# Kernel tuning notes

Measured on AMD Instinct MI355X. Metric: run time of the kernel, lower is better.

The kernel has to match this reference:

```python
import jax, jax.numpy as jnp
import numpy as np

NUM_USERS = 100000
NUM_ITEMS = 50000
EMB = 64
NNZ = 4_800_000
N = NUM_USERS + NUM_ITEMS


def setup_inputs() -> dict:
    key = jax.random.key(0)
    k1, k2, k3, k4, k5 = jax.random.split(key, 5)
    row = jax.random.randint(k1, (NNZ,), 0, N, dtype=jnp.int64 if jax.config.jax_enable_x64 else jnp.int32)
    col = jax.random.randint(k2, (NNZ,), 0, N, dtype=row.dtype)
    # normalized adjacency values (positive, ~1/avg_degree scale)
    vals = jax.random.uniform(k3, (NNZ,), dtype=jnp.float32) * (1.0 / 32.0)
    user_emb = jax.random.normal(k4, (NUM_USERS, EMB), dtype=jnp.float32)
    item_emb = jax.random.normal(k5, (NUM_ITEMS, EMB), dtype=jnp.float32)
    return {"row": row, "col": col, "vals": vals,
            "user_emb": user_emb, "item_emb": item_emb, "n_layers": 3}


def reference(row, col, vals, user_emb, item_emb, n_layers):
    # ego_embeddings = cat(user, item)  -> [N, D]
    ego = jnp.concatenate([user_emb, item_emb], axis=0)
    acc = ego  # running sum over layers (layer 0 included)
    for _ in range(n_layers):
        # sparse.mm(norm_adj, ego): gather source rows, scale, scatter-add to dest rows
        ego = jax.ops.segment_sum(vals[:, None] * ego[col], row, num_segments=N)
        acc = acc + ego
    mean_emb = acc / jnp.asarray(n_layers + 1, dtype=acc.dtype)  # mean over layer axis
    return mean_emb[:NUM_USERS], mean_emb[NUM_USERS:]
```

## Files before the change

kernel.cpp:

```cpp
#include <hip/hip_runtime.h>
#include <hip/hip_fp16.h>


#define NUSERS 100000
#define NITEMS 50000
#define NN     150000
#define D      64
#define NNZ_E  4800000

#define NB_BU  586
#define BU_PAD 592
#define NCHUNK 1024
#define CH     4688
#define STAGE_CAP 16384

__global__ void init_kernel(const float* __restrict__ ue,
                            const float* __restrict__ ie,
                            float* __restrict__ acc,
                            __half* __restrict__ ego) {
    int t = blockIdx.x * blockDim.x + threadIdx.x;
    const int total = NN * (D / 4);
    if (t >= total) return;
    const int user_f4 = NUSERS * (D / 4);
    float4 v;
    if (t < user_f4) v = ((const float4*)ue)[t];
    else             v = ((const float4*)ie)[t - user_f4];
    ((float4*)acc)[t] = v;
    __half2 h01 = __float22half2_rn(make_float2(v.x, v.y));
    __half2 h23 = __float22half2_rn(make_float2(v.z, v.w));
    uint2 packed;
    packed.x = *(unsigned*)&h01;
    packed.y = *(unsigned*)&h23;
    ((uint2*)ego)[t] = packed;
}

__global__ void p1_kernel(const int* __restrict__ row, int* __restrict__ cnt) {
    __shared__ int l[BU_PAD];
    for (int i = threadIdx.x; i < BU_PAD; i += 256) l[i] = 0;
    __syncthreads();
    int b = blockIdx.x;
    int beg = b * CH, end = min(beg + CH, NNZ_E);
    for (int e = beg + threadIdx.x; e < end; e += 256)
        atomicAdd(&l[row[e] >> 8], 1);
    __syncthreads();
    for (int i = threadIdx.x; i < BU_PAD; i += 256) cnt[b * BU_PAD + i] = l[i];
}

__global__ void s1_kernel(const int* __restrict__ cnt,
                          int* __restrict__ woff,
                          int* __restrict__ butot) {
    __shared__ int wsum[16];
    int bu = blockIdx.x;
    int c = threadIdx.x;
    int lane = c & 63;
    int w = c >> 6;
    int d = cnt[c * BU_PAD + bu];
    int incl = d;
    #pragma unroll
    for (int off = 1; off < 64; off <<= 1) {
        int t = __shfl_up(incl, off, 64);
        if (lane >= off) incl += t;
    }
    if (lane == 63) wsum[w] = incl;
    __syncthreads();
    int woffs = 0;
    for (int i = 0; i < w; ++i) woffs += wsum[i];
    woff[c * BU_PAD + bu] = woffs + incl - d;
    if (c == 1023) butot[bu] = woffs + incl;
}

__global__ void s2_kernel(const int* __restrict__ butot, int* __restrict__ bbase) {
    __shared__ int sh[1024];
    int t = threadIdx.x;
    sh[t] = (t < NB_BU) ? butot[t] : 0;
    __syncthreads();
    for (int off = 1; off < 1024; off <<= 1) {
        int x = (t >= off) ? sh[t - off] : 0;
        __syncthreads();
        sh[t] += x;
        __syncthreads();
    }
    if (t == 0) bbase[0] = 0;
    if (t < NB_BU) bbase[t + 1] = sh[t];
}

__global__ void p2_kernel(const int* __restrict__ row,
                          const int* __restrict__ col,
                          const float* __restrict__ vals,
                          const int* __restrict__ woff,
                          const int* __restrict__ bbase,
                          uint2* __restrict__ rec) {
    __shared__ int cur[BU_PAD];
    int b = blockIdx.x;
    for (int i = threadIdx.x; i < BU_PAD; i += 256) {
        int base = (i < NB_BU) ? bbase[i] : 0;
        cur[i] = base + woff[b * BU_PAD + i];
    }
    __syncthreads();
    int beg = b * CH, end = min(beg + CH, NNZ_E);
    for (int e = beg + threadIdx.x; e < end; e += 256) {
        int r = row[e];
        unsigned code = (unsigned)(vals[e] * 524288.0f + 0.5f);
        code = min(code, 16383u);
        unsigned cv = ((unsigned)col[e] << 14) | code;
        int p = atomicAdd(&cur[r >> 8], 1);
        rec[p] = make_uint2(cv, (unsigned)(r & 255));
    }
}

__global__ __launch_bounds__(512) void p3f_kernel(const int* __restrict__ bbase,
                                                  const uint2* __restrict__ rec,
                                                  int* __restrict__ start,
                                                  int* __restrict__ deg,
                                                  unsigned* __restrict__ ecv) {
    __shared__ unsigned stage[STAGE_CAP];
    __shared__ int lh[256];
    __shared__ int cur[256];
    __shared__ int wsum[4];
    int bu = blockIdx.x;
    int beg = bbase[bu], end = bbase[bu + 1];
    int t = threadIdx.x;
    if (t < 256) lh[t] = 0;
    __syncthreads();
    for (int i = beg + t; i < end; i += 512)
        atomicAdd(&lh[rec[i].y], 1);
    __syncthreads();
    int h = 0, incl = 0;
    int lane = t & 63, w = t >> 6;
    if (t < 256) {
        h = lh[t];
        incl = h;
        #pragma unroll
        for (int off = 1; off < 64; off <<= 1) {
            int x = __shfl_up(incl, off, 64);
            if (lane >= off) incl += x;
        }
        if (lane == 63) wsum[w] = incl;
    }
    __syncthreads();
    if (t < 256) {
        int woffs = 0;
        for (int i = 0; i < w; ++i) woffs += wsum[i];
        int excl = woffs + incl - h;
        cur[t] = excl;
        int n0 = (bu << 8) + t;
        if (n0 < NN) {
            start[n0] = beg + excl;
            deg[n0] = h;
        }
    }
    __syncthreads();
    for (int i = beg + t; i < end; i += 512) {
        uint2 r = rec[i];
        int p = atomicAdd(&cur[r.y], 1);
        stage[p] = r.x;
    }
    __syncthreads();
    int n_edges = end - beg;
    for (int i = t; i < n_edges; i += 512)
        ecv[beg + i] = stage[i];
}

#define STEP(rj, cj) do {                                              \
    float v_ = (float)((cj) & 16383u) * (1.0f / 524288.0f);            \
    const __half* h_ = (const __half*)&(rj);                           \
    sum[0] = fmaf(v_, __half2float(h_[0]), sum[0]);                    \
    sum[1] = fmaf(v_, __half2float(h_[1]), sum[1]);                    \
    sum[2] = fmaf(v_, __half2float(h_[2]), sum[2]);                    \
    sum[3] = fmaf(v_, __half2float(h_[3]), sum[3]);                    \
    sum[4] = fmaf(v_, __half2float(h_[4]), sum[4]);                    \
    sum[5] = fmaf(v_, __half2float(h_[5]), sum[5]);                    \
    sum[6] = fmaf(v_, __half2float(h_[6]), sum[6]);                    \
    sum[7] = fmaf(v_, __half2float(h_[7]), sum[7]);                    \
} while (0)

__global__ void gather_kernel(const int* __restrict__ start,
                              const int* __restrict__ deg,
                              const unsigned* __restrict__ ecv,
                              const __half* __restrict__ ego,
                              __half* __restrict__ nxt,
                              float* __restrict__ acc,
                              float s, int write_next) {
    int wid = threadIdx.x >> 6;
    int lane = threadIdx.x & 63;
    int n = blockIdx.x * 4 + wid;
    int st = start[n];
    int dg = deg[n];
    int k = lane & 7;
    int g = lane >> 3;
    const float4* ego4 = (const float4*)ego;
    float sum[8] = {0.f, 0.f, 0.f, 0.f, 0.f, 0.f, 0.f, 0.f};

    for (int b = 0; b < dg; b += 64) {
        unsigned cv = (b + lane < dg) ? ecv[st + b + lane] : 0u;
        int m = min(64, dg - b);
        int steps = (m + 7) >> 3;

        for (int j = 0; j < steps; j += 2) {
            unsigned ca = (unsigned)__shfl((int)cv, 8 * j + g, 64);
            unsigned cb = (unsigned)__shfl((int)cv, 8 * j + 8 + g, 64);
            float4 ra = ego4[(ca >> 14) * 8 + k];
            float4 rb = ego4[(cb >> 14) * 8 + k];
            STEP(ra, ca);
            STEP(rb, cb);
        }
    }

    #pragma unroll
    for (int off = 8; off < 64; off <<= 1) {
        #pragma unroll
        for (int i = 0; i < 8; ++i) sum[i] += __shfl_xor(sum[i], off, 64);
    }
    if (g < 2) {
        float4 sv = (g == 0) ? make_float4(sum[0], sum[1], sum[2], sum[3])
                             : make_float4(sum[4], sum[5], sum[6], sum[7]);
        int o = n * 16 + 2 * k + g;
        float4 a = ((float4*)acc)[o];
        a.x = (a.x + sv.x) * s;
        a.y = (a.y + sv.y) * s;
        a.z = (a.z + sv.z) * s;
        a.w = (a.w + sv.w) * s;
        ((float4*)acc)[o] = a;
    }
    if (write_next && g == 0) {
        __half2 h0 = __float22half2_rn(make_float2(sum[0], sum[1]));
        __half2 h1 = __float22half2_rn(make_float2(sum[2], sum[3]));
        __half2 h2 = __float22half2_rn(make_float2(sum[4], sum[5]));
        __half2 h3 = __float22half2_rn(make_float2(sum[6], sum[7]));
        uint4 packed;
        packed.x = *(unsigned*)&h0;
        packed.y = *(unsigned*)&h1;
        packed.z = *(unsigned*)&h2;
        packed.w = *(unsigned*)&h3;
        ((uint4*)nxt)[n * 8 + k] = packed;
    }
}

extern "C" void kernel_launch(void* const* d_in, const int* in_sizes, int n_in,
                              void* d_out, int out_size, void* d_ws, size_t ws_size,
                              hipStream_t stream) {
    const int*   row  = (const int*)d_in[0];
    const int*   col  = (const int*)d_in[1];
    const float* vals = (const float*)d_in[2];
    const float* ue   = (const float*)d_in[3];
    const float* ie   = (const float*)d_in[4];

    float* acc = (float*)d_out;

    char* ws = (char*)d_ws;
    __half*   ego     = (__half*)(ws);
    __half*   nxt     = (__half*)(ws + (size_t)NN * D * 2);
    int*      cnt     = (int*)nxt;
    int*      woff    = cnt + (size_t)NCHUNK * BU_PAD;
    char*     p       = ws + 2 * (size_t)NN * D * 2;
    int*      start   = (int*)(p);              p += (size_t)NN * 4;
    int*      deg     = (int*)(p);              p += (size_t)NN * 4;
    int*      butot   = (int*)(p);              p += BU_PAD * 4;
    int*      bbase   = (int*)(p);              p += (BU_PAD + 8) * 4;
    unsigned* ecv     = (unsigned*)(p);         p += (size_t)NNZ_E * 4;
    uint2*    rec     = (uint2*)(p);

    const int f4_total = NN * (D / 4);
    const int init_blocks = (f4_total + 255) / 256;
    init_kernel<<<init_blocks, 256, 0, stream>>>(ue, ie, acc, ego);

    p1_kernel<<<NCHUNK, 256, 0, stream>>>(row, cnt);
    s1_kernel<<<NB_BU, 1024, 0, stream>>>(cnt, woff, butot);
    s2_kernel<<<1, 1024, 0, stream>>>(butot, bbase);
    p2_kernel<<<NCHUNK, 256, 0, stream>>>(row, col, vals, woff, bbase, rec);
    p3f_kernel<<<NB_BU, 512, 0, stream>>>(bbase, rec, start, deg, ecv);

    const int gather_blocks = NN / 4;
    __half* in  = ego;
    __half* out = nxt;
    for (int layer = 0; layer < 3; ++layer) {
        float s = (layer == 2) ? 0.25f : 1.0f;
        int write_next = (layer < 2) ? 1 : 0;
        gather_kernel<<<gather_blocks, 256, 0, stream>>>(start, deg, ecv, in, out, acc,
                                                         s, write_next);
        __half* tmp = in; in = out; out = tmp;
    }
}
```

Measured before the change: 542.9 us.

## Coarsen global row buckets to 1024 rows and split fine sort per 256-row sub-bucket

```diff
diff --git a/kernel.cpp b/kernel.cpp
--- a/kernel.cpp
+++ b/kernel.cpp
@@ -8,8 +8,9 @@
 #define D      64
 #define NNZ_E  4800000
 
-#define NB_BU  586
-#define BU_PAD 592
+#define NB_C   147
+#define C_PAD  160
+#define NB_F   586
 #define NCHUNK 1024
 #define CH     4688
 #define STAGE_CAP 16384
@@ -35,15 +36,15 @@
 }
 
 __global__ void p1_kernel(const int* __restrict__ row, int* __restrict__ cnt) {
-    __shared__ int l[BU_PAD];
-    for (int i = threadIdx.x; i < BU_PAD; i += 256) l[i] = 0;
+    __shared__ int l[C_PAD];
+    for (int i = threadIdx.x; i < C_PAD; i += 256) l[i] = 0;
     __syncthreads();
     int b = blockIdx.x;
     int beg = b * CH, end = min(beg + CH, NNZ_E);
     for (int e = beg + threadIdx.x; e < end; e += 256)
-        atomicAdd(&l[row[e] >> 8], 1);
-    __syncthreads();
-    for (int i = threadIdx.x; i < BU_PAD; i += 256) cnt[b * BU_PAD + i] = l[i];
+        atomicAdd(&l[row[e] >> 10], 1);
+    __syncthreads();
+    for (int i = threadIdx.x; i < C_PAD; i += 256) cnt[b * C_PAD + i] = l[i];
 }
 
 __global__ void s1_kernel(const int* __restrict__ cnt,
@@ -54,7 +55,7 @@
     int c = threadIdx.x;
     int lane = c & 63;
     int w = c >> 6;
-    int d = cnt[c * BU_PAD + bu];
+    int d = cnt[c * C_PAD + bu];
     int incl = d;
     #pragma unroll
     for (int off = 1; off < 64; off <<= 1) {
@@ -65,23 +66,23 @@
     __syncthreads();
     int woffs = 0;
     for (int i = 0; i < w; ++i) woffs += wsum[i];
-    woff[c * BU_PAD + bu] = woffs + incl - d;
+    woff[c * C_PAD + bu] = woffs + incl - d;
     if (c == 1023) butot[bu] = woffs + incl;
 }
 
 __global__ void s2_kernel(const int* __restrict__ butot, int* __restrict__ bbase) {
-    __shared__ int sh[1024];
+    __shared__ int sh[256];
     int t = threadIdx.x;
-    sh[t] = (t < NB_BU) ? butot[t] : 0;
-    __syncthreads();
-    for (int off = 1; off < 1024; off <<= 1) {
+    sh[t] = (t < NB_C) ? butot[t] : 0;
+    __syncthreads();
+    for (int off = 1; off < 256; off <<= 1) {
         int x = (t >= off) ? sh[t - off] : 0;
         __syncthreads();
         sh[t] += x;
         __syncthreads();
     }
     if (t == 0) bbase[0] = 0;
-    if (t < NB_BU) bbase[t + 1] = sh[t];
+    if (t < NB_C) bbase[t + 1] = sh[t];
 }
 
 __global__ void p2_kernel(const int* __restrict__ row,
@@ -90,11 +91,11 @@
                           const int* __restrict__ woff,
                           const int* __restrict__ bbase,
                           uint2* __restrict__ rec) {
-    __shared__ int cur[BU_PAD];
+    __shared__ int cur[C_PAD];
     int b = blockIdx.x;
-    for (int i = threadIdx.x; i < BU_PAD; i += 256) {
-        int base = (i < NB_BU) ? bbase[i] : 0;
-        cur[i] = base + woff[b * BU_PAD + i];
+    for (int i = threadIdx.x; i < C_PAD; i += 256) {
+        int base = (i < NB_C) ? bbase[i] : 0;
+        cur[i] = base + woff[b * C_PAD + i];
     }
     __syncthreads();
     int beg = b * CH, end = min(beg + CH, NNZ_E);
@@ -103,8 +104,8 @@
         unsigned code = (unsigned)(vals[e] * 524288.0f + 0.5f);
         code = min(code, 16383u);
         unsigned cv = ((unsigned)col[e] << 14) | code;
-        int p = atomicAdd(&cur[r >> 8], 1);
-        rec[p] = make_uint2(cv, (unsigned)(r & 255));
+        int p = atomicAdd(&cur[r >> 10], 1);
+        rec[p] = make_uint2(cv, (unsigned)(r & 1023));
     }
 }
 
@@ -117,16 +118,34 @@
     __shared__ int lh[256];
     __shared__ int cur[256];
     __shared__ int wsum[4];
-    int bu = blockIdx.x;
-    int beg = bbase[bu], end = bbase[bu + 1];
+    __shared__ int bsum[8];
+    int f = blockIdx.x;
+    int c = f >> 2;
+    int s = f & 3;
+    int beg = bbase[c], end = bbase[c + 1];
+    int ylo = s << 8;
     int t = threadIdx.x;
+    int lane = t & 63, w = t >> 6;
     if (t < 256) lh[t] = 0;
     __syncthreads();
-    for (int i = beg + t; i < end; i += 512)
-        atomicAdd(&lh[rec[i].y], 1);
-    __syncthreads();
+
+    int mybelow = 0;
+    for (int i = beg + t; i < end; i += 512) {
+        int y = (int)rec[i].y;
+        if ((y >> 8) == s) atomicAdd(&lh[y & 255], 1);
+        mybelow += (y < ylo) ? 1 : 0;
+    }
+    #pragma unroll
+    for (int off = 32; off >= 1; off >>= 1)
+        mybelow += __shfl_xor(mybelow, off, 64);
+    if (lane == 0) bsum[w] = mybelow;
+    __syncthreads();
+    int below = 0;
+    #pragma unroll
+    for (int i = 0; i < 8; ++i) below += bsum[i];
+    int fbase = beg + below;
+
     int h = 0, incl = 0;
-    int lane = t & 63, w = t >> 6;
     if (t < 256) {
         h = lh[t];
         incl = h;
@@ -143,22 +162,25 @@
         for (int i = 0; i < w; ++i) woffs += wsum[i];
         int excl = woffs + incl - h;
         cur[t] = excl;
-        int n0 = (bu << 8) + t;
+        int n0 = (f << 8) + t;
         if (n0 < NN) {
-            start[n0] = beg + excl;
+            start[n0] = fbase + excl;
             deg[n0] = h;
         }
     }
     __syncthreads();
+    int nf = wsum[0] + wsum[1] + wsum[2] + wsum[3];
+
     for (int i = beg + t; i < end; i += 512) {
         uint2 r = rec[i];
-        int p = atomicAdd(&cur[r.y], 1);
-        stage[p] = r.x;
-    }
-    __syncthreads();
-    int n_edges = end - beg;
-    for (int i = t; i < n_edges; i += 512)
-        ecv[beg + i] = stage[i];
+        if (((int)r.y >> 8) == s) {
+            int p = atomicAdd(&cur[r.y & 255], 1);
+            stage[p] = r.x;
+        }
+    }
+    __syncthreads();
+    for (int i = t; i < nf; i += 512)
+        ecv[fbase + i] = stage[i];
 }
 
 #define STEP(rj, cj) do {                                              \
@@ -251,12 +273,12 @@
     __half*   ego     = (__half*)(ws);
     __half*   nxt     = (__half*)(ws + (size_t)NN * D * 2);
     int*      cnt     = (int*)nxt;
-    int*      woff    = cnt + (size_t)NCHUNK * BU_PAD;
+    int*      woff    = cnt + (size_t)NCHUNK * C_PAD;
     char*     p       = ws + 2 * (size_t)NN * D * 2;
     int*      start   = (int*)(p);              p += (size_t)NN * 4;
     int*      deg     = (int*)(p);              p += (size_t)NN * 4;
-    int*      butot   = (int*)(p);              p += BU_PAD * 4;
-    int*      bbase   = (int*)(p);              p += (BU_PAD + 8) * 4;
+    int*      butot   = (int*)(p);              p += C_PAD * 4;
+    int*      bbase   = (int*)(p);              p += (C_PAD + 8) * 4;
     unsigned* ecv     = (unsigned*)(p);         p += (size_t)NNZ_E * 4;
     uint2*    rec     = (uint2*)(p);
 
@@ -265,10 +287,10 @@
     init_kernel<<<init_blocks, 256, 0, stream>>>(ue, ie, acc, ego);
 
     p1_kernel<<<NCHUNK, 256, 0, stream>>>(row, cnt);
-    s1_kernel<<<NB_BU, 1024, 0, stream>>>(cnt, woff, butot);
-    s2_kernel<<<1, 1024, 0, stream>>>(butot, bbase);
+    s1_kernel<<<NB_C, 1024, 0, stream>>>(cnt, woff, butot);
+    s2_kernel<<<1, 256, 0, stream>>>(butot, bbase);
     p2_kernel<<<NCHUNK, 256, 0, stream>>>(row, col, vals, woff, bbase, rec);
-    p3f_kernel<<<NB_BU, 512, 0, stream>>>(bbase, rec, start, deg, ecv);
+    p3f_kernel<<<NB_F, 512, 0, stream>>>(bbase, rec, start, deg, ecv);
 
     const int gather_blocks = NN / 4;
     __half* in  = ego;
```

Measured after the change: 576.5 us. 1.06x slower.

## Map one node per 8-lane group in gather and shrink CSR build chunk count

Applied to the files above, without the earlier changes.

```diff
diff --git a/kernel.cpp b/kernel.cpp
--- a/kernel.cpp
+++ b/kernel.cpp
@@ -8,10 +8,10 @@
 #define D      64
 #define NNZ_E  4800000
 
-#define NB_BU  586
+#define NB_F   586
 #define BU_PAD 592
-#define NCHUNK 1024
-#define CH     4688
+#define NCHUNK 128
+#define CH     37500
 #define STAGE_CAP 16384
 
 __global__ void init_kernel(const float* __restrict__ ue,
@@ -36,20 +36,20 @@
 
 __global__ void p1_kernel(const int* __restrict__ row, int* __restrict__ cnt) {
     __shared__ int l[BU_PAD];
-    for (int i = threadIdx.x; i < BU_PAD; i += 256) l[i] = 0;
+    for (int i = threadIdx.x; i < BU_PAD; i += 1024) l[i] = 0;
     __syncthreads();
     int b = blockIdx.x;
     int beg = b * CH, end = min(beg + CH, NNZ_E);
-    for (int e = beg + threadIdx.x; e < end; e += 256)
+    for (int e = beg + threadIdx.x; e < end; e += 1024)
         atomicAdd(&l[row[e] >> 8], 1);
     __syncthreads();
-    for (int i = threadIdx.x; i < BU_PAD; i += 256) cnt[b * BU_PAD + i] = l[i];
+    for (int i = threadIdx.x; i < BU_PAD; i += 1024) cnt[b * BU_PAD + i] = l[i];
 }
 
 __global__ void s1_kernel(const int* __restrict__ cnt,
                           int* __restrict__ woff,
                           int* __restrict__ butot) {
-    __shared__ int wsum[16];
+    __shared__ int wsum[2];
     int bu = blockIdx.x;
     int c = threadIdx.x;
     int lane = c & 63;
@@ -63,16 +63,15 @@
     }
     if (lane == 63) wsum[w] = incl;
     __syncthreads();
-    int woffs = 0;
-    for (int i = 0; i < w; ++i) woffs += wsum[i];
+    int woffs = (w == 1) ? wsum[0] : 0;
     woff[c * BU_PAD + bu] = woffs + incl - d;
-    if (c == 1023) butot[bu] = woffs + incl;
+    if (c == 127) butot[bu] = woffs + incl;
 }
 
 __global__ void s2_kernel(const int* __restrict__ butot, int* __restrict__ bbase) {
     __shared__ int sh[1024];
     int t = threadIdx.x;
-    sh[t] = (t < NB_BU) ? butot[t] : 0;
+    sh[t] = (t < NB_F) ? butot[t] : 0;
     __syncthreads();
     for (int off = 1; off < 1024; off <<= 1) {
         int x = (t >= off) ? sh[t - off] : 0;
@@ -81,7 +80,7 @@
         __syncthreads();
     }
     if (t == 0) bbase[0] = 0;
-    if (t < NB_BU) bbase[t + 1] = sh[t];
+    if (t < NB_F) bbase[t + 1] = sh[t];
 }
 
 __global__ void p2_kernel(const int* __restrict__ row,
@@ -92,13 +91,13 @@
                           uint2* __restrict__ rec) {
     __shared__ int cur[BU_PAD];
     int b = blockIdx.x;
-    for (int i = threadIdx.x; i < BU_PAD; i += 256) {
-        int base = (i < NB_BU) ? bbase[i] : 0;
+    for (int i = threadIdx.x; i < BU_PAD; i += 1024) {
+        int base = (i < NB_F) ? bbase[i] : 0;
         cur[i] = base + woff[b * BU_PAD + i];
     }
     __syncthreads();
     int beg = b * CH, end = min(beg + CH, NNZ_E);
-    for (int e = beg + threadIdx.x; e < end; e += 256) {
+    for (int e = beg + threadIdx.x; e < end; e += 1024) {
         int r = row[e];
         unsigned code = (unsigned)(vals[e] * 524288.0f + 0.5f);
         code = min(code, 16383u);
@@ -161,7 +160,7 @@
         ecv[beg + i] = stage[i];
 }
 
-#define STEP(rj, cj) do {                                              \
+#define STEPG(rj, cj) do {                                             \
     float v_ = (float)((cj) & 16383u) * (1.0f / 524288.0f);            \
     const __half* h_ = (const __half*)&(rj);                           \
     sum[0] = fmaf(v_, __half2float(h_[0]), sum[0]);                    \
@@ -183,56 +182,56 @@
                               float s, int write_next) {
     int wid = threadIdx.x >> 6;
     int lane = threadIdx.x & 63;
-    int n = blockIdx.x * 4 + wid;
-    int st = start[n];
-    int dg = deg[n];
     int k = lane & 7;
     int g = lane >> 3;
+    int n = blockIdx.x * 32 + wid * 8 + g;
     const float4* ego4 = (const float4*)ego;
     float sum[8] = {0.f, 0.f, 0.f, 0.f, 0.f, 0.f, 0.f, 0.f};
 
-    for (int b = 0; b < dg; b += 64) {
-        unsigned cv = (b + lane < dg) ? ecv[st + b + lane] : 0u;
-        int m = min(64, dg - b);
-        int steps = (m + 7) >> 3;
-
-        for (int j = 0; j < steps; j += 2) {
-            unsigned ca = (unsigned)__shfl((int)cv, 8 * j + g, 64);
-            unsigned cb = (unsigned)__shfl((int)cv, 8 * j + 8 + g, 64);
-            float4 ra = ego4[(ca >> 14) * 8 + k];
-            float4 rb = ego4[(cb >> 14) * 8 + k];
-            STEP(ra, ca);
-            STEP(rb, cb);
+    int st = 0, dg = 0;
+    if (n < NN) { st = start[n]; dg = deg[n]; }
+
+    for (int e = 0; e < dg; e += 4) {
+        unsigned c0 = ecv[st + e];
+        unsigned c1 = (e + 1 < dg) ? ecv[st + e + 1] : 0u;
+        unsigned c2 = (e + 2 < dg) ? ecv[st + e + 2] : 0u;
+        unsigned c3 = (e + 3 < dg) ? ecv[st + e + 3] : 0u;
+        float4 r0 = ego4[(c0 >> 14) * 8 + k];
+        float4 r1 = ego4[(c1 >> 14) * 8 + k];
+        float4 r2 = ego4[(c2 >> 14) * 8 + k];
+        float4 r3 = ego4[(c3 >> 14) * 8 + k];
+        STEPG(r0, c0);
+        STEPG(r1, c1);
+        STEPG(r2, c2);
+        STEPG(r3, c3);
+    }
+
+    if (n < NN) {
+        int o = n * 16 + 2 * k;
+        float4 a0 = ((float4*)acc)[o];
+        float4 a1 = ((float4*)acc)[o + 1];
+        a0.x = (a0.x + sum[0]) * s;
+        a0.y = (a0.y + sum[1]) * s;
+        a0.z = (a0.z + sum[2]) * s;
+        a0.w = (a0.w + sum[3]) * s;
+        a1.x = (a1.x + sum[4]) * s;
+        a1.y = (a1.y + sum[5]) * s;
+        a1.z = (a1.z + sum[6]) * s;
+        a1.w = (a1.w + sum[7]) * s;
+        ((float4*)acc)[o] = a0;
+        ((float4*)acc)[o + 1] = a1;
+        if (write_next) {
+            __half2 h0 = __float22half2_rn(make_float2(sum[0], sum[1]));
+            __half2 h1 = __float22half2_rn(make_float2(sum[2], sum[3]));
+            __half2 h2 = __float22half2_rn(make_float2(sum[4], sum[5]));
+            __half2 h3 = __float22half2_rn(make_float2(sum[6], sum[7]));
+            uint4 packed;
+            packed.x = *(unsigned*)&h0;
+            packed.y = *(unsigned*)&h1;
+            packed.z = *(unsigned*)&h2;
+            packed.w = *(unsigned*)&h3;
+            ((uint4*)nxt)[n * 8 + k] = packed;
         }
-    }
-
-    #pragma unroll
-    for (int off = 8; off < 64; off <<= 1) {
-        #pragma unroll
-        for (int i = 0; i < 8; ++i) sum[i] += __shfl_xor(sum[i], off, 64);
-    }
-    if (g < 2) {
-        float4 sv = (g == 0) ? make_float4(sum[0], sum[1], sum[2], sum[3])
-                             : make_float4(sum[4], sum[5], sum[6], sum[7]);
-        int o = n * 16 + 2 * k + g;
-        float4 a = ((float4*)acc)[o];
-        a.x = (a.x + sv.x) * s;
-        a.y = (a.y + sv.y) * s;
-        a.z = (a.z + sv.z) * s;
-        a.w = (a.w + sv.w) * s;
-        ((float4*)acc)[o] = a;
-    }
-    if (write_next && g == 0) {
-        __half2 h0 = __float22half2_rn(make_float2(sum[0], sum[1]));
-        __half2 h1 = __float22half2_rn(make_float2(sum[2], sum[3]));
-        __half2 h2 = __float22half2_rn(make_float2(sum[4], sum[5]));
-        __half2 h3 = __float22half2_rn(make_float2(sum[6], sum[7]));
-        uint4 packed;
-        packed.x = *(unsigned*)&h0;
-        packed.y = *(unsigned*)&h1;
-        packed.z = *(unsigned*)&h2;
-        packed.w = *(unsigned*)&h3;
-        ((uint4*)nxt)[n * 8 + k] = packed;
     }
 }
 
@@ -256,7 +255,7 @@
     int*      start   = (int*)(p);              p += (size_t)NN * 4;
     int*      deg     = (int*)(p);              p += (size_t)NN * 4;
     int*      butot   = (int*)(p);              p += BU_PAD * 4;
-    int*      bbase   = (int*)(p);              p += (BU_PAD + 8) * 4;
+    int*      bbase   = (int*)(p);              p += (NB_F + 8) * 4;
     unsigned* ecv     = (unsigned*)(p);         p += (size_t)NNZ_E * 4;
     uint2*    rec     = (uint2*)(p);
 
@@ -264,13 +263,13 @@
     const int init_blocks = (f4_total + 255) / 256;
     init_kernel<<<init_blocks, 256, 0, stream>>>(ue, ie, acc, ego);
 
-    p1_kernel<<<NCHUNK, 256, 0, stream>>>(row, cnt);
-    s1_kernel<<<NB_BU, 1024, 0, stream>>>(cnt, woff, butot);
+    p1_kernel<<<NCHUNK, 1024, 0, stream>>>(row, cnt);
+    s1_kernel<<<NB_F, 128, 0, stream>>>(cnt, woff, butot);
     s2_kernel<<<1, 1024, 0, stream>>>(butot, bbase);
-    p2_kernel<<<NCHUNK, 256, 0, stream>>>(row, col, vals, woff, bbase, rec);
-    p3f_kernel<<<NB_BU, 512, 0, stream>>>(bbase, rec, start, deg, ecv);
-
-    const int gather_blocks = NN / 4;
+    p2_kernel<<<NCHUNK, 1024, 0, stream>>>(row, col, vals, woff, bbase, rec);
+    p3f_kernel<<<NB_F, 512, 0, stream>>>(bbase, rec, start, deg, ecv);
+
+    const int gather_blocks = (NN + 31) / 32;
     __half* in  = ego;
     __half* out = nxt;
     for (int layer = 0; layer < 3; ++layer) {
```

Result: slower. 555.0 us (+2.2%).
